# Kernel optimization log

Hardware: AMD Instinct MI355X
Metric: run time of the kernel (lower is better)

The kernel has to match this reference:

```python
import jax, jax.numpy as jnp
import numpy as np

NUM_QUBITS = 24
GATE_QUBITS = 4
NUM_STEPS = 8
GATE_DIM = 2 ** GATE_QUBITS  # 16


def setup_inputs() -> dict:
    key = jax.random.key(0)
    k1, k2 = jax.random.split(key)
    # statevector: leading dim 2 = (real, imag), then one size-2 axis per qubit
    state = jax.random.normal(k1, (2,) + (2,) * NUM_QUBITS, dtype=jnp.float32)
    # gates: [steps, 2(re/im), 2^k, 2^k]
    gates = jax.random.normal(k2, (NUM_STEPS, 2, GATE_DIM, GATE_DIM), dtype=jnp.float32)
    # distinct qubit indices per step (static permutation metadata)
    rng = np.random.default_rng(0)
    targets = np.stack(
        [rng.choice(NUM_QUBITS, size=GATE_QUBITS, replace=False) for _ in range(NUM_STEPS)]
    ).astype(np.int64)
    return {"state": state, "targets": targets, "gates": gates}


def _apply_gates(state, gates, targets):
    n = NUM_QUBITS
    dims = list(range(n))
    for step in range(targets.shape[0]):
        target = [int(q) for q in targets[step]]
        # qubit q lives on axis (n-1-q) of the qubit block; reversed as in source
        target_axes = list(reversed([n - 1 - q for q in target]))
        perm = [i for i in dims if i not in target_axes] + target_axes
        perm = [0] + [i + 1 for i in perm]  # keep re/im axis in front
        inv_perm = [0] * (n + 1)
        for i, d in enumerate(perm):
            inv_perm[d] = i
        # gather target qubits into the last axis, flatten the rest
        s = jnp.transpose(state, perm).reshape(2, -1, GATE_DIM)
        sr, si = s[0], s[1]
        gr, gi = gates[step, 0], gates[step, 1]
        # complex matmul: state @ gate^T, (a+bi)(c+di) split into re/im
        nr = sr @ gr.T - si @ gi.T
        ni = sr @ gi.T + si @ gr.T
        state = jnp.transpose(
            jnp.stack([nr, ni]).reshape((2,) + (2,) * n), inv_perm
        )
    return state


def reference(state, targets, gates):
    return _apply_gates(state, gates, np.asarray(targets))
```

## Files before the change

kernel.cpp:

```cpp
#include <hip/hip_runtime.h>

#define N_QUBITS 24
#define NSTATE (1u << N_QUBITS)
#define GDIM 16
#define TILE_BITS 12
#define TILE (1u << TILE_BITS)

__global__ __launch_bounds__(256) void apply_gate4(
    const float* __restrict__ src, float* __restrict__ dst,
    const int* __restrict__ targets_raw,
    const float* __restrict__ gates,
    int step)
{
    __shared__ float gsh[2 * GDIM * GDIM];
    __shared__ float ldsR[TILE];
    __shared__ float ldsI[TILE];
    __shared__ int s12sh[12];
    __shared__ int possh[4];
    __shared__ int ntpossh[8];

    const int tid = threadIdx.x;

    const float* G = gates + (size_t)step * 512;
    gsh[2 * tid]     = G[tid];
    gsh[2 * tid + 1] = G[256 + tid];

    if (tid == 0) {
        bool is64 = true;
        for (int i = 0; i < 32; ++i) {
            if (targets_raw[2 * i + 1] != 0) { is64 = false; break; }
        }
        int t[4];
        unsigned tmask = 0;
        #pragma unroll
        for (int j = 0; j < 4; ++j) {
            t[j] = is64 ? targets_raw[2 * (step * 4 + j)]
                        : targets_raw[step * 4 + j];
            tmask |= 1u << t[j];
        }
        unsigned smask = tmask;
        int cnt = 0;
        for (int b = 0; b < N_QUBITS && cnt < 8; ++b)
            if (!((tmask >> b) & 1u)) { smask |= 1u << b; ++cnt; }
        int k = 0, k2 = 0;
        for (int b = 0; b < N_QUBITS; ++b) {
            if ((smask >> b) & 1u) {
                s12sh[k] = b;
                if (!((tmask >> b) & 1u)) ntpossh[k2++] = k;
                ++k;
            }
        }
        #pragma unroll
        for (int j = 0; j < 4; ++j)
            possh[j] = __popc(smask & ((1u << t[j]) - 1u));
    }
    __syncthreads();

    unsigned base = blockIdx.x;
    #pragma unroll
    for (int i = 0; i < 12; ++i) {
        const unsigned s = (unsigned)s12sh[i];
        base = ((base >> s) << (s + 1)) | (base & ((1u << s) - 1u));
    }
    const unsigned sh8 = s12sh[8], sh9 = s12sh[9],
                   sh10 = s12sh[10], sh11 = s12sh[11];

    unsigned addr4[4], w4[4];
    #pragma unroll
    for (int p = 0; p < 4; ++p) {
        const unsigned a = (unsigned)(tid * 4 + p * 1024);
        addr4[p] = base
                 | (a & 255u)
                 | (((a >> 8) & 1u) << sh8)
                 | (((a >> 9) & 1u) << sh9)
                 | (((a >> 10) & 1u) << sh10)
                 | (((a >> 11) & 1u) << sh11);
        w4[p] = a ^ (((a >> 5) & 7u) << 2);
    }

    #pragma unroll
    for (int p = 0; p < 4; ++p) {
        *(float4*)(ldsR + w4[p]) = *(const float4*)(src + addr4[p]);
        *(float4*)(ldsI + w4[p]) = *(const float4*)(src + NSTATE + addr4[p]);
    }
    __syncthreads();

    unsigned gb = 0;
    #pragma unroll
    for (int i = 0; i < 8; ++i)
        gb |= (((unsigned)tid >> i) & 1u) << ntpossh[i];
    const int p0 = possh[0], p1 = possh[1], p2 = possh[2], p3 = possh[3];

    unsigned aa[GDIM];
    float sr[GDIM], si[GDIM];
    #pragma unroll
    for (int h = 0; h < GDIM; ++h) {
        const unsigned a = gb
            | (((unsigned)h & 1u) << p0)
            | ((((unsigned)h >> 1) & 1u) << p1)
            | ((((unsigned)h >> 2) & 1u) << p2)
            | ((((unsigned)h >> 3) & 1u) << p3);
        const unsigned w = a ^ (((a >> 5) & 7u) << 2);
        aa[h] = w;
        sr[h] = ldsR[w];
        si[h] = ldsI[w];
    }
    #pragma unroll
    for (int g = 0; g < GDIM; ++g) {
        float ar = 0.f, ai = 0.f;
        #pragma unroll
        for (int h = 0; h < GDIM; ++h) {
            const float gr = gsh[2 * (g * GDIM + h)];
            const float gi = gsh[2 * (g * GDIM + h) + 1];
            ar = fmaf(gr, sr[h], ar);
            ar = fmaf(-gi, si[h], ar);
            ai = fmaf(gr, si[h], ai);
            ai = fmaf(gi, sr[h], ai);
        }
        ldsR[aa[g]] = ar;
        ldsI[aa[g]] = ai;
    }
    __syncthreads();

    #pragma unroll
    for (int p = 0; p < 4; ++p) {
        *(float4*)(dst + addr4[p])          = *(const float4*)(ldsR + w4[p]);
        *(float4*)(dst + NSTATE + addr4[p]) = *(const float4*)(ldsI + w4[p]);
    }
}

extern "C" void kernel_launch(void* const* d_in, const int* in_sizes, int n_in,
                              void* d_out, int out_size, void* d_ws, size_t ws_size,
                              hipStream_t stream) {
    const float* state   = (const float*)d_in[0];
    const int*   targets = (const int*)d_in[1];
    const float* gates   = (const float*)d_in[2];
    float* out = (float*)d_out;

    const dim3 block(256);
    const dim3 grid(NSTATE / TILE);

    apply_gate4<<<grid, block, 0, stream>>>(state, out, targets, gates, 0);
    for (int s = 1; s < 8; ++s) {
        apply_gate4<<<grid, block, 0, stream>>>(out, out, targets, gates, s);
    }
}
```

Before: 580.5 us.

## Fuse consecutive gate steps into shared tile sweeps via a device-side plan

A planning kernel greedily groups consecutive gate steps whose combined target qubits fit in a 13-qubit LDS tile. Each sweep then applies several gates to the tile held in shared memory before writing it back. This cuts full-statevector passes from eight to at most four, roughly halving global memory traffic. The cost is more LDS, 512-thread blocks, a changed swizzle, and extra per-gate index computation and barriers. It also adds a dead leftover kernel and fixes the number of sweeps at four, which assumes the plan never needs more groups.

```diff
diff --git a/kernel.cpp b/kernel.cpp
--- a/kernel.cpp
+++ b/kernel.cpp
@@ -1,131 +1,227 @@
 #include <hip/hip_runtime.h>
 
-#define N_QUBITS 24
-#define NSTATE (1u << N_QUBITS)
-#define GDIM 16
-#define TILE_BITS 12
-#define TILE (1u << TILE_BITS)
-
-__global__ __launch_bounds__(256) void apply_gate4(
+#define NQ 24
+#define NSTATE (1u << NQ)
+#define TB 13
+#define TILE (1u << TB)
+#define NTHR 512
+#define MAXG 4
+#define GROUP_STRIDE 80
+
+
+__global__ void plan_kernel(const int* __restrict__ targets_raw, int* __restrict__ meta)
+{
+    if (threadIdx.x != 0 || blockIdx.x != 0) return;
+    bool is64 = true;
+    for (int i = 0; i < 4; ++i)
+        if (targets_raw[2 * i + 1] != 0) { is64 = false; break; }
+
+    int t[8][4];
+    unsigned tm[8];
+    for (int s = 0; s < 8; ++s) {
+        unsigned m = 0;
+        for (int j = 0; j < 4; ++j) {
+            int v = is64 ? targets_raw[2 * (s * 4 + j)] : targets_raw[s * 4 + j];
+            t[s][j] = v; m |= 1u << v;
+        }
+        tm[s] = m;
+    }
+
+    int ng = 0, sp = 0;
+    while (sp < 8) {
+        unsigned mask = 0xFu;
+        int cnt = 0, steps[MAXG];
+        while (sp < 8 && cnt < MAXG) {
+            unsigned nm = mask | tm[sp];
+            if (__popc(nm) <= TB) { mask = nm; steps[cnt++] = sp++; }
+            else break;
+        }
+        unsigned sm = mask;
+        int need = TB - __popc(sm);
+        for (int b = 0; b < NQ && need > 0; ++b)
+            if (!((sm >> b) & 1u)) { sm |= 1u << b; --need; }
+
+        int* g = meta + 8 + ng * GROUP_STRIDE;
+        g[0] = cnt;
+        int spos[NQ];
+        int si = 0, ci = 0;
+        for (int b = 0; b < NQ; ++b) {
+            if ((sm >> b) & 1u) { spos[b] = si; g[1 + si] = b; ++si; }
+            else                { spos[b] = -1; g[14 + ci] = b; ++ci; }
+        }
+        for (int k = 0; k < cnt; ++k) {
+            int st = steps[k];
+            int* gk = g + 25 + k * 5;
+            gk[0] = st;
+            for (int j = 0; j < 4; ++j) gk[1 + j] = spos[t[st][j]];
+        }
+        ++ng;
+    }
+    meta[0] = ng;
+}
+
+__device__ __forceinline__ unsigned swz(unsigned a) {
+    return a ^ (((((a >> 5) ^ (a >> 8) ^ (a >> 11)) & 7u)) << 2);
+}
+
+__global__ __launch_bounds__(NTHR, 4) void sweep_kernel(
     const float* __restrict__ src, float* __restrict__ dst,
-    const int* __restrict__ targets_raw,
-    const float* __restrict__ gates,
-    int step)
+    const int* __restrict__ meta, int sweep)
 {
-    __shared__ float gsh[2 * GDIM * GDIM];
+    if (sweep >= meta[0]) return;
+
     __shared__ float ldsR[TILE];
     __shared__ float ldsI[TILE];
-    __shared__ int s12sh[12];
-    __shared__ int possh[4];
-    __shared__ int ntpossh[8];
+    __shared__ float gsh[MAXG][512];
+    __shared__ int s13[13], c11[11], gpos[MAXG][4], gstep[MAXG];
+    __shared__ int ngat_sh;
 
     const int tid = threadIdx.x;
-
-    const float* G = gates + (size_t)step * 512;
-    gsh[2 * tid]     = G[tid];
-    gsh[2 * tid + 1] = G[256 + tid];
-
-    if (tid == 0) {
-        bool is64 = true;
-        for (int i = 0; i < 32; ++i) {
-            if (targets_raw[2 * i + 1] != 0) { is64 = false; break; }
-        }
-        int t[4];
-        unsigned tmask = 0;
-        #pragma unroll
-        for (int j = 0; j < 4; ++j) {
-            t[j] = is64 ? targets_raw[2 * (step * 4 + j)]
-                        : targets_raw[step * 4 + j];
-            tmask |= 1u << t[j];
-        }
-        unsigned smask = tmask;
-        int cnt = 0;
-        for (int b = 0; b < N_QUBITS && cnt < 8; ++b)
-            if (!((tmask >> b) & 1u)) { smask |= 1u << b; ++cnt; }
-        int k = 0, k2 = 0;
-        for (int b = 0; b < N_QUBITS; ++b) {
-            if ((smask >> b) & 1u) {
-                s12sh[k] = b;
-                if (!((tmask >> b) & 1u)) ntpossh[k2++] = k;
-                ++k;
+    const int* g = meta + 8 + sweep * GROUP_STRIDE;
+
+    if (tid < 13) s13[tid] = g[1 + tid];
+    else if (tid >= 16 && tid < 27) c11[tid - 16] = g[14 + (tid - 16)];
+    else if (tid == 27) ngat_sh = g[0];
+    else if (tid >= 32 && tid < 32 + MAXG * 5) {
+        int k = (tid - 32) / 5, f = (tid - 32) % 5;
+        if (f == 0) gstep[k] = g[25 + k * 5];
+        else gpos[k][f - 1] = g[25 + k * 5 + f];
+    }
+    __syncthreads();
+
+    const int ngat = ngat_sh;
+    const float* gates = (const float*)0;
+    (void)gates;
+
+    unsigned base = blockIdx.x;
+    #pragma unroll
+    for (int i = 0; i < TB; ++i) {
+        const unsigned s = (unsigned)s13[i];
+        base = ((base >> s) << (s + 1)) | (base & ((1u << s) - 1u));
+    }
+    unsigned ga[4], wa[4];
+    #pragma unroll
+    for (int p = 0; p < 4; ++p) {
+        unsigned a = (unsigned)(p * 2048 + tid * 4);
+        wa[p] = swz(a);
+        unsigned spd = a;
+        #pragma unroll
+        for (int i = 0; i < 11; ++i) {
+            const unsigned c = (unsigned)c11[i];
+            spd = ((spd >> c) << (c + 1)) | (spd & ((1u << c) - 1u));
+        }
+        ga[p] = base | spd;
+    }
+    return;
+}
+
+__global__ __launch_bounds__(NTHR, 4) void sweep_full(
+    const float* __restrict__ src, float* __restrict__ dst,
+    const float* __restrict__ gates_g,
+    const int* __restrict__ meta, int sweep)
+{
+    if (sweep >= meta[0]) return;
+
+    __shared__ float ldsR[TILE];
+    __shared__ float ldsI[TILE];
+    __shared__ float gsh[MAXG][512];
+    __shared__ int s13[13], c11[11], gpos[MAXG][4], gstep[MAXG];
+    __shared__ int ngat_sh;
+
+    const int tid = threadIdx.x;
+    const int* g = meta + 8 + sweep * GROUP_STRIDE;
+
+    if (tid < 13) s13[tid] = g[1 + tid];
+    else if (tid >= 16 && tid < 27) c11[tid - 16] = g[14 + (tid - 16)];
+    else if (tid == 27) ngat_sh = g[0];
+    else if (tid >= 32 && tid < 32 + MAXG * 5) {
+        int k = (tid - 32) / 5, f = (tid - 32) % 5;
+        if (f == 0) gstep[k] = g[25 + k * 5];
+        else gpos[k][f - 1] = g[25 + k * 5 + f];
+    }
+    __syncthreads();
+
+    const int ngat = ngat_sh;
+
+    for (int k = 0; k < ngat; ++k) {
+        const float* G = gates_g + (size_t)gstep[k] * 512;
+        gsh[k][tid] = G[(tid & 1) * 256 + (tid >> 1)];
+    }
+
+    unsigned base = blockIdx.x;
+    #pragma unroll
+    for (int i = 0; i < TB; ++i) {
+        const unsigned s = (unsigned)s13[i];
+        base = ((base >> s) << (s + 1)) | (base & ((1u << s) - 1u));
+    }
+    unsigned ga[4], wa[4];
+    #pragma unroll
+    for (int p = 0; p < 4; ++p) {
+        unsigned a = (unsigned)(p * 2048 + tid * 4);
+        wa[p] = swz(a);
+        unsigned spd = a;
+        #pragma unroll
+        for (int i = 0; i < 11; ++i) {
+            const unsigned c = (unsigned)c11[i];
+            spd = ((spd >> c) << (c + 1)) | (spd & ((1u << c) - 1u));
+        }
+        ga[p] = base | spd;
+    }
+
+    #pragma unroll
+    for (int p = 0; p < 4; ++p) {
+        *(float4*)(ldsR + wa[p]) = *(const float4*)(src + ga[p]);
+        *(float4*)(ldsI + wa[p]) = *(const float4*)(src + NSTATE + ga[p]);
+    }
+    __syncthreads();
+
+    for (int k = 0; k < ngat; ++k) {
+        const int p0 = gpos[k][0], p1 = gpos[k][1], p2 = gpos[k][2], p3 = gpos[k][3];
+        const unsigned tmask = (1u << p0) | (1u << p1) | (1u << p2) | (1u << p3);
+        unsigned gb = 0;
+        {
+            int bi = 0;
+            for (int pos = 0; pos < TB; ++pos)
+                if (!((tmask >> pos) & 1u)) { gb |= (((unsigned)tid >> bi) & 1u) << pos; ++bi; }
+        }
+        unsigned aa[16];
+        float sr[16], si[16];
+        #pragma unroll
+        for (int h = 0; h < 16; ++h) {
+            const unsigned a = gb
+                | (((unsigned)h & 1u) << p0)
+                | ((((unsigned)h >> 1) & 1u) << p1)
+                | ((((unsigned)h >> 2) & 1u) << p2)
+                | ((((unsigned)h >> 3) & 1u) << p3);
+            const unsigned w = swz(a);
+            aa[h] = w;
+            sr[h] = ldsR[w];
+            si[h] = ldsI[w];
+        }
+        const float* gk = gsh[k];
+        #pragma unroll
+        for (int go = 0; go < 16; ++go) {
+            const float* row = gk + go * 32;
+            float ar = 0.f, ai = 0.f;
+            #pragma unroll
+            for (int h2 = 0; h2 < 8; ++h2) {
+                const float4 q = *(const float4*)(row + h2 * 4);
+                const int h = h2 * 2;
+                ar = fmaf(q.x, sr[h], ar);  ar = fmaf(-q.y, si[h], ar);
+                ai = fmaf(q.x, si[h], ai);  ai = fmaf(q.y, sr[h], ai);
+                ar = fmaf(q.z, sr[h + 1], ar);  ar = fmaf(-q.w, si[h + 1], ar);
+                ai = fmaf(q.z, si[h + 1], ai);  ai = fmaf(q.w, sr[h + 1], ai);
             }
-        }
-        #pragma unroll
-        for (int j = 0; j < 4; ++j)
-            possh[j] = __popc(smask & ((1u << t[j]) - 1u));
-    }
-    __syncthreads();
-
-    unsigned base = blockIdx.x;
-    #pragma unroll
-    for (int i = 0; i < 12; ++i) {
-        const unsigned s = (unsigned)s12sh[i];
-        base = ((base >> s) << (s + 1)) | (base & ((1u << s) - 1u));
-    }
-    const unsigned sh8 = s12sh[8], sh9 = s12sh[9],
-                   sh10 = s12sh[10], sh11 = s12sh[11];
-
-    unsigned addr4[4], w4[4];
-    #pragma unroll
-    for (int p = 0; p < 4; ++p) {
-        const unsigned a = (unsigned)(tid * 4 + p * 1024);
-        addr4[p] = base
-                 | (a & 255u)
-                 | (((a >> 8) & 1u) << sh8)
-                 | (((a >> 9) & 1u) << sh9)
-                 | (((a >> 10) & 1u) << sh10)
-                 | (((a >> 11) & 1u) << sh11);
-        w4[p] = a ^ (((a >> 5) & 7u) << 2);
-    }
-
-    #pragma unroll
-    for (int p = 0; p < 4; ++p) {
-        *(float4*)(ldsR + w4[p]) = *(const float4*)(src + addr4[p]);
-        *(float4*)(ldsI + w4[p]) = *(const float4*)(src + NSTATE + addr4[p]);
-    }
-    __syncthreads();
-
-    unsigned gb = 0;
-    #pragma unroll
-    for (int i = 0; i < 8; ++i)
-        gb |= (((unsigned)tid >> i) & 1u) << ntpossh[i];
-    const int p0 = possh[0], p1 = possh[1], p2 = possh[2], p3 = possh[3];
-
-    unsigned aa[GDIM];
-    float sr[GDIM], si[GDIM];
-    #pragma unroll
-    for (int h = 0; h < GDIM; ++h) {
-        const unsigned a = gb
-            | (((unsigned)h & 1u) << p0)
-            | ((((unsigned)h >> 1) & 1u) << p1)
-            | ((((unsigned)h >> 2) & 1u) << p2)
-            | ((((unsigned)h >> 3) & 1u) << p3);
-        const unsigned w = a ^ (((a >> 5) & 7u) << 2);
-        aa[h] = w;
-        sr[h] = ldsR[w];
-        si[h] = ldsI[w];
-    }
-    #pragma unroll
-    for (int g = 0; g < GDIM; ++g) {
-        float ar = 0.f, ai = 0.f;
-        #pragma unroll
-        for (int h = 0; h < GDIM; ++h) {
-            const float gr = gsh[2 * (g * GDIM + h)];
-            const float gi = gsh[2 * (g * GDIM + h) + 1];
-            ar = fmaf(gr, sr[h], ar);
-            ar = fmaf(-gi, si[h], ar);
-            ai = fmaf(gr, si[h], ai);
-            ai = fmaf(gi, sr[h], ai);
-        }
-        ldsR[aa[g]] = ar;
-        ldsI[aa[g]] = ai;
-    }
-    __syncthreads();
-
-    #pragma unroll
-    for (int p = 0; p < 4; ++p) {
-        *(float4*)(dst + addr4[p])          = *(const float4*)(ldsR + w4[p]);
-        *(float4*)(dst + NSTATE + addr4[p]) = *(const float4*)(ldsI + w4[p]);
+            ldsR[aa[go]] = ar;
+            ldsI[aa[go]] = ai;
+        }
+        __syncthreads();
+    }
+
+    #pragma unroll
+    for (int p = 0; p < 4; ++p) {
+        *(float4*)(dst + ga[p])          = *(const float4*)(ldsR + wa[p]);
+        *(float4*)(dst + NSTATE + ga[p]) = *(const float4*)(ldsI + wa[p]);
     }
 }
 
@@ -136,12 +232,14 @@
     const int*   targets = (const int*)d_in[1];
     const float* gates   = (const float*)d_in[2];
     float* out = (float*)d_out;
-
-    const dim3 block(256);
+    int* meta = (int*)d_ws;
+
+    plan_kernel<<<1, 64, 0, stream>>>(targets, meta);
+
+    const dim3 block(NTHR);
     const dim3 grid(NSTATE / TILE);
 
-    apply_gate4<<<grid, block, 0, stream>>>(state, out, targets, gates, 0);
-    for (int s = 1; s < 8; ++s) {
-        apply_gate4<<<grid, block, 0, stream>>>(out, out, targets, gates, s);
-    }
-}
+    sweep_full<<<grid, block, 0, stream>>>(state, out, gates, meta, 0);
+    for (int s = 1; s < MAXG; ++s)
+        sweep_full<<<grid, block, 0, stream>>>(out, out, gates, meta, s);
+}
```

Result: faster. 519.6 us (-10.5%).
